# Optimization experiments

Measured on AMD Instinct MI355X. Metric: run time of the kernel, lower is better.

The kernel has to match this reference:

```python
import jax, jax.numpy as jnp
import numpy as np


def setup_inputs() -> dict:
    key = jax.random.key(0)
    ks = jax.random.split(key, 7)
    B, EN, DE, E, U, T = 8, 512, 64, 512, 512, 100  # batch, max_words, max_label, emb, units, topics
    return {
        "en_seq": jax.random.normal(ks[0], (B, EN, E), dtype=jnp.float32),
        "de_seq": jax.random.normal(ks[1], (B, DE, E), dtype=jnp.float32),
        "topics": jax.random.uniform(ks[2], (B, T), dtype=jnp.float32),
        "w_en": jax.random.normal(ks[3], (E, U), dtype=jnp.float32) * 0.05,
        "w_de": jax.random.normal(ks[4], (E, U), dtype=jnp.float32) * 0.05,
        "nu": jax.random.normal(ks[5], (U,), dtype=jnp.float32) * 0.05,
        "wt": jax.random.normal(ks[6], (E, T), dtype=jnp.float32) * 0.05,
    }


def reference(en_seq, de_seq, topics, w_en, w_de, nu, wt):
    # Additive (Bahdanau-style) attention with a per-batch topic bias.
    att_en = jnp.einsum("bie,eu->biu", en_seq, w_en)        # [B, EN, U]
    att_de = jnp.einsum("bje,eu->bju", de_seq, w_de)        # [B, DE, U]
    topics_w = jnp.einsum("bt,ut->bu", topics, wt)          # [B, U] (wt is [E,U-dim? no: E==U])
    # co_m[b, j, i, u] = att_en[b,i,u] + att_de[b,j,u] + topics_w[b,u]
    co_m = jnp.tanh(att_en[:, None, :, :] + att_de[:, :, None, :]
                    + topics_w[:, None, None, :])           # [B, DE, EN, U]
    mu = jnp.einsum("bjiu,u->bji", co_m, nu)                # [B, DE, EN]
    alphas = jax.nn.softmax(mu, axis=-1)                    # softmax over encoder positions
    p_gen = jax.nn.sigmoid(mu)
    sum_en = jnp.einsum("bji,bie->bje", alphas, en_seq)     # attention-weighted encoder sum
    output = de_seq + sum_en
    return (output, alphas, p_gen)
```

## Files before the change

kernel.cpp:

```cpp
#include <hip/hip_runtime.h>
#include <hip/hip_bf16.h>

#define NB  8
#define ENW 512
#define DEW 64
#define EMB 512
#define UN  512
#define NT  100

#define KSCALE 2.8853900817779268f
#define L2E    1.4426950408889634f

typedef short bf16x8 __attribute__((ext_vector_type(8)));
typedef unsigned short u16x8 __attribute__((ext_vector_type(8)));
typedef float f32x4  __attribute__((ext_vector_type(4)));

#define GLOAD_LDS16(src, dst) __builtin_amdgcn_global_load_lds( \
    (const __attribute__((address_space(1))) void*)(src),       \
    (__attribute__((address_space(3))) void*)(dst), 16, 0, 0)

__device__ __forceinline__ unsigned short f2bf(float f) {
    union { float f; unsigned int u; } v; v.f = f;
    unsigned int r = v.u + 0x7FFFu + ((v.u >> 16) & 1u);
    return (unsigned short)(r >> 16);
}

__global__ __launch_bounds__(256) void prep_kernel(const float* __restrict__ w_en,
                                                   const float* __restrict__ w_de,
                                                   const float* __restrict__ en,
                                                   const float* __restrict__ de,
                                                   const float* __restrict__ topics,
                                                   const float* __restrict__ wt_mat,
                                                   const float* __restrict__ nu,
                                                   unsigned short* __restrict__ wen_t,
                                                   unsigned short* __restrict__ wde_t,
                                                   unsigned short* __restrict__ en_bf,
                                                   unsigned short* __restrict__ de_bf,
                                                   float* __restrict__ tw2,
                                                   float* __restrict__ snu,
                                                   float* __restrict__ nu2) {
    const int bx = blockIdx.x, t = threadIdx.x;
    if (bx < 128) {
        __shared__ float tile[64][65];
        const float* w = (bx < 64) ? w_en : w_de;
        unsigned short* o = (bx < 64) ? wen_t : wde_t;
        const int tb = bx & 63;
        const int r0 = (tb >> 3) * 64;
        const int c0 = (tb & 7) * 64;
        const int rr = t >> 4, cc = (t & 15) * 4;
#pragma unroll
        for (int q = 0; q < 4; ++q) {
            float4 v = *(const float4*)(w + (size_t)(r0 + rr + 16 * q) * 512 + c0 + cc);
            *(float4*)&tile[rr + 16 * q][cc] = v;
        }
        __syncthreads();
#pragma unroll
        for (int q = 0; q < 4; ++q) {
            int ul = rr + 16 * q;
            int el = cc;
            ushort4 v;
            v.x = f2bf(KSCALE * tile[el][ul]);
            v.y = f2bf(KSCALE * tile[el + 1][ul]);
            v.z = f2bf(KSCALE * tile[el + 2][ul]);
            v.w = f2bf(KSCALE * tile[el + 3][ul]);
            *(ushort4*)(o + (size_t)(c0 + ul) * 512 + r0 + el) = v;
        }
    } else if (bx < 1280) {
        const bool is_en = (bx < 1152);
        const float* src = is_en ? en : de;
        unsigned short* dst = is_en ? en_bf : de_bf;
        const int idx = ((is_en ? (bx - 128) : (bx - 1152)) * 256 + t) * 8;
        float4 a0 = *(const float4*)(src + idx);
        float4 a1 = *(const float4*)(src + idx + 4);
        u16x8 o;
        o[0] = f2bf(a0.x); o[1] = f2bf(a0.y); o[2] = f2bf(a0.z); o[3] = f2bf(a0.w);
        o[4] = f2bf(a1.x); o[5] = f2bf(a1.y); o[6] = f2bf(a1.z); o[7] = f2bf(a1.w);
        *(u16x8*)(dst + idx) = o;
    } else if (bx < 1296) {
        int idx = (bx - 1280) * 256 + t;
        int b = idx >> 9, u = idx & 511;
        const float* tp = topics + b * NT;
        const float* wp = wt_mat + u * NT;
        float s = 0.f;
        for (int tt = 0; tt < NT; ++tt) s += tp[tt] * wp[tt];
        tw2[idx] = KSCALE * s;
    } else {
        __shared__ float red[256];
        float n0 = nu[t], n1 = nu[t + 256];
        nu2[t] = -2.f * n0;
        nu2[t + 256] = -2.f * n1;
        red[t] = n0 + n1;
        __syncthreads();
        for (int off = 128; off > 0; off >>= 1) {
            if (t < off) red[t] += red[t + off];
            __syncthreads();
        }
        if (t == 0) snu[0] = red[0];
    }
}

__global__ __launch_bounds__(256) void gemm_fused(const unsigned short* __restrict__ en_bf,
                                                  const unsigned short* __restrict__ de_bf,
                                                  const unsigned short* __restrict__ wen_t,
                                                  const unsigned short* __restrict__ wde_t,
                                                  const float* __restrict__ tw2,
                                                  float* __restrict__ Ea,
                                                  float* __restrict__ Eb) {
    __shared__ unsigned short Blds[64 * 512];
    const int K = 512, N = 512;
    const int bx = blockIdx.x;
    const bool is_de = (bx >= 64);
    const unsigned short* A = is_de ? de_bf : en_bf;
    const unsigned short* Bt = is_de ? wde_t : wen_t;
    float* C = is_de ? Eb : Ea;
    const int mb = is_de ? (bx - 64) : bx;

    const int lane = threadIdx.x & 63;
    const int wave = threadIdx.x >> 6;
    const int n0 = blockIdx.y * 64;

#pragma unroll
    for (int q = 0; q < 16; ++q) {
        const int R = wave * 16 + q;
        const unsigned short* src = Bt + (size_t)(n0 + R) * K + ((lane * 8) ^ ((R & 7) << 3));
        GLOAD_LDS16(src, &Blds[R * 512]);
    }

    const int m0 = mb * 64 + wave * 16;
    const int row = m0 + (lane & 15);
    const int kq  = (lane >> 4) * 8;
    const int nrow = lane & 15;
    const int swz = (nrow & 7) << 3;

    f32x4 acc[4];
#pragma unroll
    for (int nn = 0; nn < 4; ++nn) acc[nn] = 0.f;

    const unsigned short* ap = A + (size_t)row * K + kq;
    bf16x8 apre[4];
#pragma unroll
    for (int q = 0; q < 4; ++q) apre[q] = *(const bf16x8*)(ap + q * 32);

    __syncthreads();
#pragma unroll
    for (int g = 0; g < 4; ++g) {
        bf16x8 acur[4];
#pragma unroll
        for (int q = 0; q < 4; ++q) acur[q] = apre[q];
        if (g < 3) {
#pragma unroll
            for (int q = 0; q < 4; ++q) apre[q] = *(const bf16x8*)(ap + (g + 1) * 128 + q * 32);
        }
#pragma unroll
        for (int q = 0; q < 4; ++q) {
            const int kc = g * 128 + q * 32;
            const int col = (kq + kc) ^ swz;
#pragma unroll
            for (int nn = 0; nn < 4; ++nn) {
                bf16x8 b = *(const bf16x8*)&Blds[(nrow + nn * 16) * 512 + col];
                acc[nn] = __builtin_amdgcn_mfma_f32_16x16x32_bf16(acur[q], b, acc[nn], 0, 0, 0);
            }
        }
    }
    const int crow = m0 + (lane >> 4) * 4;
    const int ccol = lane & 15;
#pragma unroll
    for (int nn = 0; nn < 4; ++nn)
#pragma unroll
        for (int r = 0; r < 4; ++r) {
            int rw = crow + r, cl = n0 + nn * 16 + ccol;
            float v = acc[nn][r];
            if (is_de) v += tw2[(rw >> 6) * 512 + cl];
            C[(size_t)rw * N + cl] = __builtin_amdgcn_exp2f(v);
        }
}

__global__ __launch_bounds__(256) void mu5_kernel(const float* __restrict__ Ea,
                                                  const float* __restrict__ Eb,
                                                  const float* __restrict__ nu2,
                                                  float* __restrict__ mu0,
                                                  float* __restrict__ mu1) {
    __shared__ float As[64][132];
    __shared__ float Bs[16][132];
    const int t = threadIdx.x;
    const int bx = blockIdx.x;
    const int us = bx & 1;
    const int it = (bx >> 1) & 7;
    const int jt = (bx >> 4) & 3;
    const int b  = bx >> 6;
    const int i0 = it * 64, j0 = jt * 16, u0 = us * 256;
    const int il = t & 15, jr = t >> 4;

    const float* aeb = Ea + (size_t)(b * ENW + i0) * UN;
    const float* beb = Eb + (size_t)(b * DEW + j0) * UN;

    float s0 = 0.f, s1 = 0.f, s2 = 0.f, s3 = 0.f;
#pragma unroll
    for (int half = 0; half < 2; ++half) {
        const int uc = u0 + half * 128;
#pragma unroll
        for (int q = 0; q < 8; ++q) {
            int idx = q * 256 + t;
            int rowi = idx >> 5, c4 = idx & 31;
            *(float4*)&As[rowi][c4 * 4] = *(const float4*)(aeb + (size_t)rowi * UN + uc + c4 * 4);
        }
#pragma unroll
        for (int q = 0; q < 2; ++q) {
            int idx = q * 256 + t;
            int rowi = idx >> 5, c4 = idx & 31;
            *(float4*)&Bs[rowi][c4 * 4] = *(const float4*)(beb + (size_t)rowi * UN + uc + c4 * 4);
        }
        __syncthreads();
#pragma unroll 8
        for (int c = 0; c < 32; ++c) {
            float4 bb = *(const float4*)&Bs[jr][c * 4];
            float4 nv = *(const float4*)(nu2 + uc + c * 4);
            float4 a0 = *(const float4*)&As[il][c * 4];
            float4 a1 = *(const float4*)&As[il + 16][c * 4];
            float4 a2 = *(const float4*)&As[il + 32][c * 4];
            float4 a3 = *(const float4*)&As[il + 48][c * 4];
            {
                float q0 = fmaf(a0.x, bb.x, 1.f), q1 = fmaf(a0.y, bb.y, 1.f);
                float q2 = fmaf(a0.z, bb.z, 1.f), q3 = fmaf(a0.w, bb.w, 1.f);
                float dA = q0 * q1, dB = q2 * q3;
                float nA = fmaf(nv.y, q0, nv.x * q1);
                float nB = fmaf(nv.w, q2, nv.z * q3);
                float num = fmaf(nB, dA, nA * dB);
                s0 = fmaf(num, __builtin_amdgcn_rcpf(dA * dB), s0);
            }
            {
                float q0 = fmaf(a1.x, bb.x, 1.f), q1 = fmaf(a1.y, bb.y, 1.f);
                float q2 = fmaf(a1.z, bb.z, 1.f), q3 = fmaf(a1.w, bb.w, 1.f);
                float dA = q0 * q1, dB = q2 * q3;
                float nA = fmaf(nv.y, q0, nv.x * q1);
                float nB = fmaf(nv.w, q2, nv.z * q3);
                float num = fmaf(nB, dA, nA * dB);
                s1 = fmaf(num, __builtin_amdgcn_rcpf(dA * dB), s1);
            }
            {
                float q0 = fmaf(a2.x, bb.x, 1.f), q1 = fmaf(a2.y, bb.y, 1.f);
                float q2 = fmaf(a2.z, bb.z, 1.f), q3 = fmaf(a2.w, bb.w, 1.f);
                float dA = q0 * q1, dB = q2 * q3;
                float nA = fmaf(nv.y, q0, nv.x * q1);
                float nB = fmaf(nv.w, q2, nv.z * q3);
                float num = fmaf(nB, dA, nA * dB);
                s2 = fmaf(num, __builtin_amdgcn_rcpf(dA * dB), s2);
            }
            {
                float q0 = fmaf(a3.x, bb.x, 1.f), q1 = fmaf(a3.y, bb.y, 1.f);
                float q2 = fmaf(a3.z, bb.z, 1.f), q3 = fmaf(a3.w, bb.w, 1.f);
                float dA = q0 * q1, dB = q2 * q3;
                float nA = fmaf(nv.y, q0, nv.x * q1);
                float nB = fmaf(nv.w, q2, nv.z * q3);
                float num = fmaf(nB, dA, nA * dB);
                s3 = fmaf(num, __builtin_amdgcn_rcpf(dA * dB), s3);
            }
        }
        __syncthreads();
    }
    float* mo = us ? mu1 : mu0;
    const size_t base = (size_t)(b * DEW + j0 + jr) * ENW + i0 + il;
    mo[base]      = s0;
    mo[base + 16] = s1;
    mo[base + 32] = s2;
    mo[base + 48] = s3;
}

__global__ __launch_bounds__(256) void softfin_kernel(const float* __restrict__ mu0,
                                                      const float* __restrict__ mu1,
                                                      const float* __restrict__ snu,
                                                      const float* __restrict__ en,
                                                      const float* __restrict__ de,
                                                      float* __restrict__ out,
                                                      float* __restrict__ alphas,
                                                      float* __restrict__ p_gen) {
    __shared__ float Al[4][512];
    __shared__ float Ps[4][4][256];
    const int bx = blockIdx.x;
    const int eh = bx & 1;
    const int jq = (bx >> 1) & 15;
    const int b  = bx >> 5;
    const int t = threadIdx.x;
    const int wave = t >> 6, lane = t & 63;
    const int j0 = jq * 4;
    const float snu0 = snu[0];

    {
        const int bj = b * DEW + j0 + wave;
        const float* mup0 = mu0 + (size_t)bj * ENW;
        const float* mup1 = mu1 + (size_t)bj * ENW;
        float v[8], a[8];
#pragma unroll
        for (int c = 0; c < 8; ++c) v[c] = mup0[c * 64 + lane] + mup1[c * 64 + lane] + snu0;
        float mx = v[0];
#pragma unroll
        for (int c = 1; c < 8; ++c) mx = fmaxf(mx, v[c]);
#pragma unroll
        for (int off = 32; off > 0; off >>= 1) mx = fmaxf(mx, __shfl_xor(mx, off));
        float s = 0.f;
#pragma unroll
        for (int c = 0; c < 8; ++c) { a[c] = __builtin_amdgcn_exp2f((v[c] - mx) * L2E); s += a[c]; }
#pragma unroll
        for (int off = 32; off > 0; off >>= 1) s += __shfl_xor(s, off);
        float inv = __builtin_amdgcn_rcpf(s);
#pragma unroll
        for (int c = 0; c < 8; ++c) {
            a[c] *= inv;
            Al[wave][c * 64 + lane] = a[c];
        }
        if (eh == 0) {
            float* alp = alphas + (size_t)bj * ENW;
            float* pgp = p_gen + (size_t)bj * ENW;
#pragma unroll
            for (int c = 0; c < 8; ++c) {
                alp[c * 64 + lane] = a[c];
                pgp[c * 64 + lane] = __builtin_amdgcn_rcpf(1.f + __builtin_amdgcn_exp2f(-v[c] * L2E));
            }
        }
    }
    __syncthreads();

    const int i0 = wave * 128;
    const float* enb = en + (size_t)b * ENW * EMB + eh * 256 + lane * 4;
    f32x4 acc[4];
#pragma unroll
    for (int jj = 0; jj < 4; ++jj) acc[jj] = 0.f;
#pragma unroll 2
    for (int ig = 0; ig < 128; ig += 4) {
        const int ib = i0 + ig;
        float4 al0 = *(const float4*)&Al[0][ib];
        float4 al1 = *(const float4*)&Al[1][ib];
        float4 al2 = *(const float4*)&Al[2][ib];
        float4 al3 = *(const float4*)&Al[3][ib];
#pragma unroll
        for (int r = 0; r < 4; ++r) {
            float4 x = *(const float4*)(enb + (size_t)(ib + r) * EMB);
            float w0 = (r == 0) ? al0.x : (r == 1) ? al0.y : (r == 2) ? al0.z : al0.w;
            float w1 = (r == 0) ? al1.x : (r == 1) ? al1.y : (r == 2) ? al1.z : al1.w;
            float w2 = (r == 0) ? al2.x : (r == 1) ? al2.y : (r == 2) ? al2.z : al2.w;
            float w3 = (r == 0) ? al3.x : (r == 1) ? al3.y : (r == 2) ? al3.z : al3.w;
            acc[0][0] = fmaf(w0, x.x, acc[0][0]); acc[0][1] = fmaf(w0, x.y, acc[0][1]);
            acc[0][2] = fmaf(w0, x.z, acc[0][2]); acc[0][3] = fmaf(w0, x.w, acc[0][3]);
            acc[1][0] = fmaf(w1, x.x, acc[1][0]); acc[1][1] = fmaf(w1, x.y, acc[1][1]);
            acc[1][2] = fmaf(w1, x.z, acc[1][2]); acc[1][3] = fmaf(w1, x.w, acc[1][3]);
            acc[2][0] = fmaf(w2, x.x, acc[2][0]); acc[2][1] = fmaf(w2, x.y, acc[2][1]);
            acc[2][2] = fmaf(w2, x.z, acc[2][2]); acc[2][3] = fmaf(w2, x.w, acc[2][3]);
            acc[3][0] = fmaf(w3, x.x, acc[3][0]); acc[3][1] = fmaf(w3, x.y, acc[3][1]);
            acc[3][2] = fmaf(w3, x.z, acc[3][2]); acc[3][3] = fmaf(w3, x.w, acc[3][3]);
        }
    }
#pragma unroll
    for (int jj = 0; jj < 4; ++jj)
        *(f32x4*)&Ps[wave][jj][lane * 4] = acc[jj];
    __syncthreads();

    {
        const int bj = b * DEW + j0 + wave;
        const int e = eh * 256 + lane * 4;
        float4 p0 = *(const float4*)&Ps[0][wave][lane * 4];
        float4 p1 = *(const float4*)&Ps[1][wave][lane * 4];
        float4 p2 = *(const float4*)&Ps[2][wave][lane * 4];
        float4 p3 = *(const float4*)&Ps[3][wave][lane * 4];
        float4 d = *(const float4*)(de + (size_t)bj * EMB + e);
        float4 o;
        o.x = d.x + (p0.x + p1.x) + (p2.x + p3.x);
        o.y = d.y + (p0.y + p1.y) + (p2.y + p3.y);
        o.z = d.z + (p0.z + p1.z) + (p2.z + p3.z);
        o.w = d.w + (p0.w + p1.w) + (p2.w + p3.w);
        *(float4*)(out + (size_t)bj * EMB + e) = o;
    }
}

extern "C" void kernel_launch(void* const* d_in, const int* in_sizes, int n_in,
                              void* d_out, int out_size, void* d_ws, size_t ws_size,
                              hipStream_t stream) {
    const float* en     = (const float*)d_in[0];
    const float* de     = (const float*)d_in[1];
    const float* topics = (const float*)d_in[2];
    const float* w_en   = (const float*)d_in[3];
    const float* w_de   = (const float*)d_in[4];
    const float* nu     = (const float*)d_in[5];
    const float* wt     = (const float*)d_in[6];

    float* out    = (float*)d_out;
    float* alphas = out + 262144;
    float* p_gen  = out + 524288;

    char* ws = (char*)d_ws;
    float* Ea             = (float*)(ws);
    float* Eb             = (float*)(ws + 8388608);
    float* tw2            = (float*)(ws + 9437184);
    unsigned short* en_bf = (unsigned short*)(ws + 9453568);
    float* mu0            = (float*)(ws + 9453568);
    float* mu1            = (float*)(ws + 10502144);
    unsigned short* de_bf = (unsigned short*)(ws + 13647872);
    unsigned short* wen_t = (unsigned short*)(ws + 14172160);
    unsigned short* wde_t = (unsigned short*)(ws + 14696448);
    float* snu            = (float*)(ws + 15220736);
    float* nu2            = (float*)(ws + 15220752);

    prep_kernel<<<1297, 256, 0, stream>>>(w_en, w_de, en, de, topics, wt, nu,
                                          wen_t, wde_t, en_bf, de_bf, tw2, snu, nu2);
    gemm_fused<<<dim3(72, 8), 256, 0, stream>>>(en_bf, de_bf, wen_t, wde_t, tw2, Ea, Eb);
    mu5_kernel<<<512, 256, 0, stream>>>(Ea, Eb, nu2, mu0, mu1);
    softfin_kernel<<<256, 256, 0, stream>>>(mu0, mu1, snu, en, de, out, alphas, p_gen);
}
```

Measured before the change: 121.1 us.

## Fuse prep kernel into GEMM with on-the-fly bf16 conversion and weight transpose

Removes the separate prep kernel and does the fp32-to-bf16 conversion, scaling and transposition of the weight tiles inside the GEMM, along with the per-block topic bias. The nu scaling moves into the mu5 epilogue and the nu sum into softfin, and softfin now runs 512 threads with the encoder reduction split over 8 waves. This saves a launch and the workspace round trip. In exchange each GEMM block redundantly loads strided fp32 weight columns and converts A inline.

```diff
diff --git a/kernel.cpp b/kernel.cpp
--- a/kernel.cpp
+++ b/kernel.cpp
@@ -15,115 +15,58 @@
 typedef unsigned short u16x8 __attribute__((ext_vector_type(8)));
 typedef float f32x4  __attribute__((ext_vector_type(4)));
 
-#define GLOAD_LDS16(src, dst) __builtin_amdgcn_global_load_lds( \
-    (const __attribute__((address_space(1))) void*)(src),       \
-    (__attribute__((address_space(3))) void*)(dst), 16, 0, 0)
-
 __device__ __forceinline__ unsigned short f2bf(float f) {
     union { float f; unsigned int u; } v; v.f = f;
     unsigned int r = v.u + 0x7FFFu + ((v.u >> 16) & 1u);
     return (unsigned short)(r >> 16);
 }
 
-__global__ __launch_bounds__(256) void prep_kernel(const float* __restrict__ w_en,
-                                                   const float* __restrict__ w_de,
-                                                   const float* __restrict__ en,
-                                                   const float* __restrict__ de,
-                                                   const float* __restrict__ topics,
-                                                   const float* __restrict__ wt_mat,
-                                                   const float* __restrict__ nu,
-                                                   unsigned short* __restrict__ wen_t,
-                                                   unsigned short* __restrict__ wde_t,
-                                                   unsigned short* __restrict__ en_bf,
-                                                   unsigned short* __restrict__ de_bf,
-                                                   float* __restrict__ tw2,
-                                                   float* __restrict__ snu,
-                                                   float* __restrict__ nu2) {
-    const int bx = blockIdx.x, t = threadIdx.x;
-    if (bx < 128) {
-        __shared__ float tile[64][65];
-        const float* w = (bx < 64) ? w_en : w_de;
-        unsigned short* o = (bx < 64) ? wen_t : wde_t;
-        const int tb = bx & 63;
-        const int r0 = (tb >> 3) * 64;
-        const int c0 = (tb & 7) * 64;
-        const int rr = t >> 4, cc = (t & 15) * 4;
-#pragma unroll
-        for (int q = 0; q < 4; ++q) {
-            float4 v = *(const float4*)(w + (size_t)(r0 + rr + 16 * q) * 512 + c0 + cc);
-            *(float4*)&tile[rr + 16 * q][cc] = v;
-        }
-        __syncthreads();
-#pragma unroll
-        for (int q = 0; q < 4; ++q) {
-            int ul = rr + 16 * q;
-            int el = cc;
-            ushort4 v;
-            v.x = f2bf(KSCALE * tile[el][ul]);
-            v.y = f2bf(KSCALE * tile[el + 1][ul]);
-            v.z = f2bf(KSCALE * tile[el + 2][ul]);
-            v.w = f2bf(KSCALE * tile[el + 3][ul]);
-            *(ushort4*)(o + (size_t)(c0 + ul) * 512 + r0 + el) = v;
-        }
-    } else if (bx < 1280) {
-        const bool is_en = (bx < 1152);
-        const float* src = is_en ? en : de;
-        unsigned short* dst = is_en ? en_bf : de_bf;
-        const int idx = ((is_en ? (bx - 128) : (bx - 1152)) * 256 + t) * 8;
-        float4 a0 = *(const float4*)(src + idx);
-        float4 a1 = *(const float4*)(src + idx + 4);
-        u16x8 o;
-        o[0] = f2bf(a0.x); o[1] = f2bf(a0.y); o[2] = f2bf(a0.z); o[3] = f2bf(a0.w);
-        o[4] = f2bf(a1.x); o[5] = f2bf(a1.y); o[6] = f2bf(a1.z); o[7] = f2bf(a1.w);
-        *(u16x8*)(dst + idx) = o;
-    } else if (bx < 1296) {
-        int idx = (bx - 1280) * 256 + t;
-        int b = idx >> 9, u = idx & 511;
-        const float* tp = topics + b * NT;
-        const float* wp = wt_mat + u * NT;
+__global__ __launch_bounds__(256) void gemm_all(const float* __restrict__ en,
+                                                const float* __restrict__ de,
+                                                const float* __restrict__ w_en,
+                                                const float* __restrict__ w_de,
+                                                const float* __restrict__ topics,
+                                                const float* __restrict__ wt_mat,
+                                                float* __restrict__ Ea,
+                                                float* __restrict__ Eb) {
+    __shared__ unsigned short Blds[64 * 512];
+    __shared__ float tws[64];
+    const int N = 512;
+    const int bx = blockIdx.x;
+    const bool is_de = (bx >= 64);
+    const float* A = is_de ? de : en;
+    const float* W = is_de ? w_de : w_en;
+    float* C = is_de ? Eb : Ea;
+    const int mb = is_de ? (bx - 64) : bx;
+
+    const int t = threadIdx.x;
+    const int lane = t & 63;
+    const int wave = t >> 6;
+    const int n0 = blockIdx.y * 64;
+
+    {
+        const int u = t & 63;
+        const int q = t >> 6;
+        const int sw = (u & 7) << 3;
+        const float* wcol = W + n0 + u;
+        unsigned short* brow = &Blds[u * 512];
+#pragma unroll
+        for (int m = 0; m < 16; ++m) {
+            const int e0 = m * 32 + q * 8;
+            const float* p = wcol + (size_t)e0 * 512;
+            bf16x8 o;
+#pragma unroll
+            for (int j = 0; j < 8; ++j)
+                o[j] = (short)f2bf(KSCALE * p[(size_t)j * 512]);
+            *(bf16x8*)&brow[e0 ^ sw] = o;
+        }
+    }
+    if (is_de && t < 64) {
+        const float* tp = topics + mb * NT;
+        const float* wp = wt_mat + (size_t)(n0 + t) * NT;
         float s = 0.f;
         for (int tt = 0; tt < NT; ++tt) s += tp[tt] * wp[tt];
-        tw2[idx] = KSCALE * s;
-    } else {
-        __shared__ float red[256];
-        float n0 = nu[t], n1 = nu[t + 256];
-        nu2[t] = -2.f * n0;
-        nu2[t + 256] = -2.f * n1;
-        red[t] = n0 + n1;
-        __syncthreads();
-        for (int off = 128; off > 0; off >>= 1) {
-            if (t < off) red[t] += red[t + off];
-            __syncthreads();
-        }
-        if (t == 0) snu[0] = red[0];
-    }
-}
-
-__global__ __launch_bounds__(256) void gemm_fused(const unsigned short* __restrict__ en_bf,
-                                                  const unsigned short* __restrict__ de_bf,
-                                                  const unsigned short* __restrict__ wen_t,
-                                                  const unsigned short* __restrict__ wde_t,
-                                                  const float* __restrict__ tw2,
-                                                  float* __restrict__ Ea,
-                                                  float* __restrict__ Eb) {
-    __shared__ unsigned short Blds[64 * 512];
-    const int K = 512, N = 512;
-    const int bx = blockIdx.x;
-    const bool is_de = (bx >= 64);
-    const unsigned short* A = is_de ? de_bf : en_bf;
-    const unsigned short* Bt = is_de ? wde_t : wen_t;
-    float* C = is_de ? Eb : Ea;
-    const int mb = is_de ? (bx - 64) : bx;
-
-    const int lane = threadIdx.x & 63;
-    const int wave = threadIdx.x >> 6;
-    const int n0 = blockIdx.y * 64;
-
-#pragma unroll
-    for (int q = 0; q < 16; ++q) {
-        const int R = wave * 16 + q;
-        const unsigned short* src = Bt + (size_t)(n0 + R) * K + ((lane * 8) ^ ((R & 7) << 3));
-        GLOAD_LDS16(src, &Blds[R * 512]);
+        tws[t] = KSCALE * s;
     }
 
     const int m0 = mb * 64 + wave * 16;
@@ -136,29 +79,47 @@
 #pragma unroll
     for (int nn = 0; nn < 4; ++nn) acc[nn] = 0.f;
 
-    const unsigned short* ap = A + (size_t)row * K + kq;
+    const float* apf = A + (size_t)row * 512 + kq;
     bf16x8 apre[4];
 #pragma unroll
-    for (int q = 0; q < 4; ++q) apre[q] = *(const bf16x8*)(ap + q * 32);
+    for (int qq = 0; qq < 4; ++qq) {
+        float4 x0 = *(const float4*)(apf + qq * 32);
+        float4 x1 = *(const float4*)(apf + qq * 32 + 4);
+        bf16x8 o;
+        o[0] = (short)f2bf(x0.x); o[1] = (short)f2bf(x0.y);
+        o[2] = (short)f2bf(x0.z); o[3] = (short)f2bf(x0.w);
+        o[4] = (short)f2bf(x1.x); o[5] = (short)f2bf(x1.y);
+        o[6] = (short)f2bf(x1.z); o[7] = (short)f2bf(x1.w);
+        apre[qq] = o;
+    }
 
     __syncthreads();
 #pragma unroll
     for (int g = 0; g < 4; ++g) {
         bf16x8 acur[4];
 #pragma unroll
-        for (int q = 0; q < 4; ++q) acur[q] = apre[q];
+        for (int qq = 0; qq < 4; ++qq) acur[qq] = apre[qq];
         if (g < 3) {
 #pragma unroll
-            for (int q = 0; q < 4; ++q) apre[q] = *(const bf16x8*)(ap + (g + 1) * 128 + q * 32);
-        }
-#pragma unroll
-        for (int q = 0; q < 4; ++q) {
-            const int kc = g * 128 + q * 32;
+            for (int qq = 0; qq < 4; ++qq) {
+                float4 x0 = *(const float4*)(apf + (g + 1) * 128 + qq * 32);
+                float4 x1 = *(const float4*)(apf + (g + 1) * 128 + qq * 32 + 4);
+                bf16x8 o;
+                o[0] = (short)f2bf(x0.x); o[1] = (short)f2bf(x0.y);
+                o[2] = (short)f2bf(x0.z); o[3] = (short)f2bf(x0.w);
+                o[4] = (short)f2bf(x1.x); o[5] = (short)f2bf(x1.y);
+                o[6] = (short)f2bf(x1.z); o[7] = (short)f2bf(x1.w);
+                apre[qq] = o;
+            }
+        }
+#pragma unroll
+        for (int qq = 0; qq < 4; ++qq) {
+            const int kc = g * 128 + qq * 32;
             const int col = (kq + kc) ^ swz;
 #pragma unroll
             for (int nn = 0; nn < 4; ++nn) {
                 bf16x8 b = *(const bf16x8*)&Blds[(nrow + nn * 16) * 512 + col];
-                acc[nn] = __builtin_amdgcn_mfma_f32_16x16x32_bf16(acur[q], b, acc[nn], 0, 0, 0);
+                acc[nn] = __builtin_amdgcn_mfma_f32_16x16x32_bf16(acur[qq], b, acc[nn], 0, 0, 0);
             }
         }
     }
@@ -170,14 +131,14 @@
         for (int r = 0; r < 4; ++r) {
             int rw = crow + r, cl = n0 + nn * 16 + ccol;
             float v = acc[nn][r];
-            if (is_de) v += tw2[(rw >> 6) * 512 + cl];
+            if (is_de) v += tws[nn * 16 + ccol];
             C[(size_t)rw * N + cl] = __builtin_amdgcn_exp2f(v);
         }
 }
 
 __global__ __launch_bounds__(256) void mu5_kernel(const float* __restrict__ Ea,
                                                   const float* __restrict__ Eb,
-                                                  const float* __restrict__ nu2,
+                                                  const float* __restrict__ nu,
                                                   float* __restrict__ mu0,
                                                   float* __restrict__ mu1) {
     __shared__ float As[64][132];
@@ -214,7 +175,7 @@
 #pragma unroll 8
         for (int c = 0; c < 32; ++c) {
             float4 bb = *(const float4*)&Bs[jr][c * 4];
-            float4 nv = *(const float4*)(nu2 + uc + c * 4);
+            float4 nv = *(const float4*)(nu + uc + c * 4);
             float4 a0 = *(const float4*)&As[il][c * 4];
             float4 a1 = *(const float4*)&As[il + 16][c * 4];
             float4 a2 = *(const float4*)&As[il + 32][c * 4];
@@ -260,22 +221,22 @@
     }
     float* mo = us ? mu1 : mu0;
     const size_t base = (size_t)(b * DEW + j0 + jr) * ENW + i0 + il;
-    mo[base]      = s0;
-    mo[base + 16] = s1;
-    mo[base + 32] = s2;
-    mo[base + 48] = s3;
-}
-
-__global__ __launch_bounds__(256) void softfin_kernel(const float* __restrict__ mu0,
+    mo[base]      = -2.f * s0;
+    mo[base + 16] = -2.f * s1;
+    mo[base + 32] = -2.f * s2;
+    mo[base + 48] = -2.f * s3;
+}
+
+__global__ __launch_bounds__(512) void softfin_kernel(const float* __restrict__ mu0,
                                                       const float* __restrict__ mu1,
-                                                      const float* __restrict__ snu,
+                                                      const float* __restrict__ nu,
                                                       const float* __restrict__ en,
                                                       const float* __restrict__ de,
                                                       float* __restrict__ out,
                                                       float* __restrict__ alphas,
                                                       float* __restrict__ p_gen) {
     __shared__ float Al[4][512];
-    __shared__ float Ps[4][4][256];
+    __shared__ float Ps[8][4][256];
     const int bx = blockIdx.x;
     const int eh = bx & 1;
     const int jq = (bx >> 1) & 15;
@@ -283,15 +244,20 @@
     const int t = threadIdx.x;
     const int wave = t >> 6, lane = t & 63;
     const int j0 = jq * 4;
-    const float snu0 = snu[0];
-
-    {
+
+    float sn = 0.f;
+#pragma unroll
+    for (int k = 0; k < 8; ++k) sn += nu[lane + 64 * k];
+#pragma unroll
+    for (int off = 32; off > 0; off >>= 1) sn += __shfl_xor(sn, off);
+
+    if (wave < 4) {
         const int bj = b * DEW + j0 + wave;
         const float* mup0 = mu0 + (size_t)bj * ENW;
         const float* mup1 = mu1 + (size_t)bj * ENW;
         float v[8], a[8];
 #pragma unroll
-        for (int c = 0; c < 8; ++c) v[c] = mup0[c * 64 + lane] + mup1[c * 64 + lane] + snu0;
+        for (int c = 0; c < 8; ++c) v[c] = mup0[c * 64 + lane] + mup1[c * 64 + lane] + sn;
         float mx = v[0];
 #pragma unroll
         for (int c = 1; c < 8; ++c) mx = fmaxf(mx, v[c]);
@@ -320,13 +286,13 @@
     }
     __syncthreads();
 
-    const int i0 = wave * 128;
+    const int i0 = wave * 64;
     const float* enb = en + (size_t)b * ENW * EMB + eh * 256 + lane * 4;
     f32x4 acc[4];
 #pragma unroll
     for (int jj = 0; jj < 4; ++jj) acc[jj] = 0.f;
 #pragma unroll 2
-    for (int ig = 0; ig < 128; ig += 4) {
+    for (int ig = 0; ig < 64; ig += 4) {
         const int ib = i0 + ig;
         float4 al0 = *(const float4*)&Al[0][ib];
         float4 al1 = *(const float4*)&Al[1][ib];
@@ -354,19 +320,23 @@
         *(f32x4*)&Ps[wave][jj][lane * 4] = acc[jj];
     __syncthreads();
 
-    {
+    if (wave < 4) {
         const int bj = b * DEW + j0 + wave;
         const int e = eh * 256 + lane * 4;
         float4 p0 = *(const float4*)&Ps[0][wave][lane * 4];
         float4 p1 = *(const float4*)&Ps[1][wave][lane * 4];
         float4 p2 = *(const float4*)&Ps[2][wave][lane * 4];
         float4 p3 = *(const float4*)&Ps[3][wave][lane * 4];
+        float4 p4 = *(const float4*)&Ps[4][wave][lane * 4];
+        float4 p5 = *(const float4*)&Ps[5][wave][lane * 4];
+        float4 p6 = *(const float4*)&Ps[6][wave][lane * 4];
+        float4 p7 = *(const float4*)&Ps[7][wave][lane * 4];
         float4 d = *(const float4*)(de + (size_t)bj * EMB + e);
         float4 o;
-        o.x = d.x + (p0.x + p1.x) + (p2.x + p3.x);
-        o.y = d.y + (p0.y + p1.y) + (p2.y + p3.y);
-        o.z = d.z + (p0.z + p1.z) + (p2.z + p3.z);
-        o.w = d.w + (p0.w + p1.w) + (p2.w + p3.w);
+        o.x = d.x + ((p0.x + p1.x) + (p2.x + p3.x)) + ((p4.x + p5.x) + (p6.x + p7.x));
+        o.y = d.y + ((p0.y + p1.y) + (p2.y + p3.y)) + ((p4.y + p5.y) + (p6.y + p7.y));
+        o.z = d.z + ((p0.z + p1.z) + (p2.z + p3.z)) + ((p4.z + p5.z) + (p6.z + p7.z));
+        o.w = d.w + ((p0.w + p1.w) + (p2.w + p3.w)) + ((p4.w + p5.w) + (p6.w + p7.w));
         *(float4*)(out + (size_t)bj * EMB + e) = o;
     }
 }
@@ -387,21 +357,12 @@
     float* p_gen  = out + 524288;
 
     char* ws = (char*)d_ws;
-    float* Ea             = (float*)(ws);
-    float* Eb             = (float*)(ws + 8388608);
-    float* tw2            = (float*)(ws + 9437184);
-    unsigned short* en_bf = (unsigned short*)(ws + 9453568);
-    float* mu0            = (float*)(ws + 9453568);
-    float* mu1            = (float*)(ws + 10502144);
-    unsigned short* de_bf = (unsigned short*)(ws + 13647872);
-    unsigned short* wen_t = (unsigned short*)(ws + 14172160);
-    unsigned short* wde_t = (unsigned short*)(ws + 14696448);
-    float* snu            = (float*)(ws + 15220736);
-    float* nu2            = (float*)(ws + 15220752);
-
-    prep_kernel<<<1297, 256, 0, stream>>>(w_en, w_de, en, de, topics, wt, nu,
-                                          wen_t, wde_t, en_bf, de_bf, tw2, snu, nu2);
-    gemm_fused<<<dim3(72, 8), 256, 0, stream>>>(en_bf, de_bf, wen_t, wde_t, tw2, Ea, Eb);
-    mu5_kernel<<<512, 256, 0, stream>>>(Ea, Eb, nu2, mu0, mu1);
-    softfin_kernel<<<256, 256, 0, stream>>>(mu0, mu1, snu, en, de, out, alphas, p_gen);
-}
+    float* Ea  = (float*)(ws);
+    float* Eb  = (float*)(ws + 8388608);
+    float* mu0 = (float*)(ws + 9437184);
+    float* mu1 = (float*)(ws + 10485760);
+
+    gemm_all<<<dim3(72, 8), 256, 0, stream>>>(en, de, w_en, w_de, topics, wt, Ea, Eb);
+    mu5_kernel<<<512, 256, 0, stream>>>(Ea, Eb, nu, mu0, mu1);
+    softfin_kernel<<<256, 512, 0, stream>>>(mu0, mu1, nu, en, de, out, alphas, p_gen);
+}
```

Measured after the change: 121.9 us (median of 2 runs). No clear change (+0.7%).
